# Kernel tuning notes

Measured on AMD Instinct MI355X. Metric: run time of the kernel, lower is better.

## Reference

```python
import jax, jax.numpy as jnp
import numpy as np

N, G, NG, E, P, D, H, L, MPD = 2048, 16, 128, 32768, 131072, 128, 4, 2, 5
EDI, EDH, IN_D, OUT_D, FFN = 16, 64, 64, 64, 512


def setup_inputs() -> dict:
    key = jax.random.key(0)
    ks = iter(jax.random.split(key, 64))
    nk = lambda: next(ks)
    # edges: endpoints within the same graph block
    ge = jnp.arange(E) // (E // G)
    edge_index = jnp.stack([
        ge * NG + jax.random.randint(nk(), (E,), 0, NG),
        ge * NG + jax.random.randint(nk(), (E,), 0, NG)]).astype(jnp.int32)
    # unique (src,dst) pairs per graph (flattened edge_paths dict)
    PG = P // G
    perm = jax.vmap(lambda k: jax.random.permutation(k, NG * NG)[:PG])(
        jax.random.split(nk(), G))  # [G,PG]
    off = (jnp.arange(G) * NG)[:, None]
    path_src = (off + perm // NG).reshape(-1).astype(jnp.int32)
    path_dst = (off + perm % NG).reshape(-1).astype(jnp.int32)
    gp = jnp.arange(P) // PG
    path_edges = (gp[:, None] * (E // G)
                  + jax.random.randint(nk(), (P, MPD), 0, E // G)).astype(jnp.int32)
    path_lens = jax.random.randint(nk(), (P,), 1, MPD + 1).astype(jnp.int32)
    ptr = (jnp.arange(G + 1) * NG).astype(jnp.int32)
    r = lambda shape, s=1.0: jax.random.normal(nk(), shape, jnp.float32) * s
    return dict(
        x=r((N, IN_D)), edge_attr=r((E, EDI)),
        edge_index=edge_index, path_src=path_src, path_dst=path_dst,
        path_edges=path_edges, path_lens=path_lens, ptr=ptr,
        W_in=r((IN_D, D), 0.1), b_in=jnp.zeros((D,)),
        W_ein=r((EDI, EDH), 0.1), b_ein=jnp.zeros((EDH,)),
        z_in=r((64, D), 0.02), z_out=r((64, D), 0.02),
        b_spatial=r((MPD,)),
        ln1_g=jnp.ones((L, D)), ln1_b=jnp.zeros((L, D)),
        Wq=r((L, H, D, D), 0.05), bq=jnp.zeros((L, H, D)),
        Wk=r((L, H, D, D), 0.05), bk=jnp.zeros((L, H, D)),
        Wv=r((L, H, D, D), 0.05), bv=jnp.zeros((L, H, D)),
        edge_vec=r((L, H, MPD, EDH), 0.1),
        Wo=r((L, H * D, D), 0.05), bo=jnp.zeros((L, D)),
        ln2_g=jnp.ones((L, D)), ln2_b=jnp.zeros((L, D)),
        W_f1=r((L, D, FFN), 0.05), b_f1=jnp.zeros((L, FFN)),
        W_f2=r((L, FFN, D), 0.05), b_f2=jnp.zeros((L, D)),
        W_out=r((D, OUT_D), 0.05), b_out=jnp.zeros((OUT_D,)),
    )


def _ln(x, g, b, eps=1e-5):
    m = jnp.mean(x, -1, keepdims=True)
    v = jnp.mean((x - m) ** 2, -1, keepdims=True)
    return (x - m) / jnp.sqrt(v + eps) * g + b


def _graphormer(x, edge_attr, W_in, b_in, W_ein, b_ein, z_in, z_out, b_spatial,
                ln1_g, ln1_b, Wq, bq, Wk, bk, Wv, bv, edge_vec, Wo, bo,
                ln2_g, ln2_b, W_f1, b_f1, W_f2, b_f2, W_out, b_out,
                edge_index, path_src, path_dst, path_edges, path_lens, ptr):
    n = x.shape[0]
    x = x @ W_in + b_in                      # node input projection
    ea = edge_attr @ W_ein + b_ein           # edge input projection
    # centrality encoding (degrees clipped to max-1)
    in_deg = jnp.minimum(jnp.zeros((n,), jnp.int32).at[edge_index[1]].add(1), z_in.shape[0] - 1)
    out_deg = jnp.minimum(jnp.zeros((n,), jnp.int32).at[edge_index[0]].add(1), z_out.shape[0] - 1)
    x = x + z_in[in_deg] + z_out[out_deg]
    # spatial encoding matrix b[src,dst] = b_spatial[min(len, MPD)-1]
    mpd = b_spatial.shape[0]
    bmat = jnp.zeros((n, n), x.dtype).at[path_src, path_dst].set(
        b_spatial[jnp.minimum(path_lens, mpd) - 1])
    # block-diagonal batch masks from ptr
    gids = jnp.searchsorted(ptr, jnp.arange(n), side='right') - 1
    block = gids[:, None] == gids[None, :]
    mask_neg = jnp.where(block, 1.0, -1e6).astype(x.dtype)
    mask_zero = block.astype(x.dtype)
    pe = ea[path_edges]                      # [P,MPD,EDH] gathered path edge feats
    pos_mask = (jnp.arange(mpd)[None, :] < path_lens[:, None]).astype(x.dtype)
    lens_f = path_lens.astype(x.dtype)
    nl, d = Wq.shape[0], x.shape[1]
    scale = jnp.sqrt(jnp.asarray(d, x.dtype))
    for l in range(nl):
        xn = _ln(x, ln1_g[l], ln1_b[l])
        q = jnp.einsum('nd,hde->hne', xn, Wq[l]) + bq[l][:, None, :]
        k = jnp.einsum('nd,hde->hne', xn, Wk[l]) + bk[l][:, None, :]
        v = jnp.einsum('nd,hde->hne', xn, Wv[l]) + bv[l][:, None, :]
        # per-head edge encoding: mean over path of <edge_vec[i], edge_attr[path[i]]>
        dots = jnp.einsum('hme,pme->hpm', edge_vec[l], pe)   # [H,P,MPD]
        vals = jnp.nan_to_num((dots * pos_mask).sum(-1) / lens_f)  # [H,P]
        c = jnp.zeros((vals.shape[0], n, n), x.dtype).at[:, path_src, path_dst].set(vals)
        a = jnp.einsum('hne,hme->hnm', q, k) / scale
        a = a * mask_zero                     # compute_a only fills diagonal blocks
        a = (a + bmat[None] + c) * mask_neg[None]
        sm = jax.nn.softmax(a, axis=-1) * mask_zero[None]
        o = jnp.einsum('hnm,hme->hne', sm, v)  # [H,N,D]
        o = jnp.transpose(o, (1, 0, 2)).reshape(n, -1) @ Wo[l] + bo[l]
        x = o + x
        x2 = _ln(x, ln2_g[l], ln2_b[l])
        x = (jax.nn.gelu(x2 @ W_f1[l] + b_f1[l], approximate=False) @ W_f2[l] + b_f2[l]) + x
    return x @ W_out + b_out


def reference(x, edge_attr, edge_index, path_src, path_dst, path_edges, path_lens, ptr,
              W_in, b_in, W_ein, b_ein, z_in, z_out, b_spatial,
              ln1_g, ln1_b, Wq, bq, Wk, bk, Wv, bv, edge_vec, Wo, bo,
              ln2_g, ln2_b, W_f1, b_f1, W_f2, b_f2, W_out, b_out):
    return _graphormer(x, edge_attr, W_in, b_in, W_ein, b_ein, z_in, z_out, b_spatial,
                       ln1_g, ln1_b, Wq, bq, Wk, bk, Wv, bv, edge_vec, Wo, bo,
                       ln2_g, ln2_b, W_f1, b_f1, W_f2, b_f2, W_out, b_out,
                       edge_index, path_src, path_dst, path_edges, path_lens, ptr)
```

## Files before the change

### kernel.cpp

```cpp
#include <hip/hip_runtime.h>
#include <math.h>

static constexpr int N_ = 2048, NG_ = 128, E_ = 32768, P_ = 131072,
  D_ = 128, H_ = 4, L_ = 2, MPD_ = 5, EDI_ = 16, EDH_ = 64,
  IND_ = 64, OUTD_ = 64, FFN_ = 512;

__global__ void k_deg(const int* __restrict__ ei, int* __restrict__ din, int* __restrict__ dou) {
  int e = blockIdx.x * blockDim.x + threadIdx.x;
  if (e < E_) {
    atomicAdd(&dou[ei[e]], 1);
    atomicAdd(&din[ei[E_ + e]], 1);
  }
}

__global__ void k_nodeproj(const float* __restrict__ x_in, const float* __restrict__ W,
                           const float* __restrict__ b, const float* __restrict__ z_in,
                           const float* __restrict__ z_out, const int* __restrict__ din,
                           const int* __restrict__ dou, float* __restrict__ x) {
  int n = blockIdx.x;
  int d = threadIdx.x;
  __shared__ float xs[IND_];
  if (d < IND_) xs[d] = x_in[n * IND_ + d];
  __syncthreads();
  float acc = b[d];
  for (int i = 0; i < IND_; ++i) acc += xs[i] * W[i * D_ + d];
  int di = min(din[n], 63), dz = min(dou[n], 63);
  acc += z_in[di * D_ + d] + z_out[dz * D_ + d];
  x[n * D_ + d] = acc;
}

__global__ void k_eproj(const float* __restrict__ ein, const float* __restrict__ W,
                        const float* __restrict__ b, float* __restrict__ ea) {
  int idx = blockIdx.x * blockDim.x + threadIdx.x;
  int e = idx >> 6, c = idx & 63;
  const float* row = ein + e * EDI_;
  float acc = b[c];
  for (int i = 0; i < EDI_; ++i) acc += row[i] * W[i * EDH_ + c];
  ea[idx] = acc;
}

static constexpr int ED_PAD = EDH_ + 4;
__global__ __launch_bounds__(256)
void k_edot2(const float* __restrict__ evec, const float* __restrict__ ea,
             float* __restrict__ edot) {
  __shared__ float eas[64][ED_PAD];
  __shared__ float evs[40][ED_PAD];
  int t = threadIdx.x;
  int e0 = blockIdx.x * 64;
  for (int i = t; i < 64 * (EDH_ / 4); i += 256) {
    int r = i >> 4, c = (i & 15) << 2;
    float4 v = *(const float4*)(ea + (size_t)(e0 + r) * EDH_ + c);
    *(float4*)&eas[r][c] = v;
  }
  for (int i = t; i < 40 * (EDH_ / 4); i += 256) {
    int r = i >> 4, c = (i & 15) << 2;
    float4 v = *(const float4*)(evec + (size_t)r * EDH_ + c);
    *(float4*)&evs[r][c] = v;
  }
  __syncthreads();
  int le = t & 63;
  int s0 = t >> 6;
  float acc[10];
  for (int ss = 0; ss < 10; ++ss) acc[ss] = 0.f;
  for (int i = 0; i < EDH_; i += 4) {
    float4 a = *(const float4*)&eas[le][i];
    for (int ss = 0; ss < 10; ++ss) {
      float4 b = *(const float4*)&evs[s0 + ss * 4][i];
      acc[ss] += a.x * b.x + a.y * b.y + a.z * b.z + a.w * b.w;
    }
  }
  for (int ss = 0; ss < 10; ++ss)
    edot[(size_t)(s0 + ss * 4) * E_ + e0 + le] = acc[ss];
}

__global__ void k_scatter(const int* __restrict__ psrc, const int* __restrict__ pdst,
                          const int* __restrict__ pedg, const int* __restrict__ plen,
                          const float* __restrict__ bsp, const float* __restrict__ edot_l,
                          float* __restrict__ bias) {
  int idx = blockIdx.x * blockDim.x + threadIdx.x;
  if (idx >= P_ * H_) return;
  int p = idx >> 2, h = idx & 3;
  int len = plen[p];
  int src = psrc[p];
  int dst = pdst[p] & (NG_ - 1);
  float acc = 0.f;
  for (int m = 0; m < MPD_; ++m)
    if (m < len) acc += edot_l[(h * MPD_ + m) * E_ + pedg[p * MPD_ + m]];
  float val = acc / (float)len + bsp[len - 1];
  bias[(h * N_ + src) * NG_ + dst] = val;
}

__global__ void k_ln(const float* __restrict__ x, const float* __restrict__ g,
                     const float* __restrict__ b, float* __restrict__ out) {
  int n = blockIdx.x;
  int d = threadIdx.x;
  float v = x[n * D_ + d];
  __shared__ float red[D_];
  red[d] = v; __syncthreads();
  for (int s = 64; s > 0; s >>= 1) { if (d < s) red[d] += red[d + s]; __syncthreads(); }
  float mean = red[0] * (1.0f / D_);
  __syncthreads();
  float c = v - mean;
  red[d] = c * c; __syncthreads();
  for (int s = 64; s > 0; s >>= 1) { if (d < s) red[d] += red[d + s]; __syncthreads(); }
  float var = red[0] * (1.0f / D_);
  out[n * D_ + d] = c * rsqrtf(var + 1e-5f) * g[d] + b[d];
}

static constexpr int QKV_ROWS = 8;
__global__ void k_qkv(const float* __restrict__ xn,
                      const float* __restrict__ Wq, const float* __restrict__ bq,
                      const float* __restrict__ Wk, const float* __restrict__ bk,
                      const float* __restrict__ Wv, const float* __restrict__ bv,
                      float* __restrict__ q, float* __restrict__ k, float* __restrict__ v) {
  int rb = blockIdx.x;
  int mh = blockIdx.y;
  int mat = mh >> 2, h = mh & 3;
  int e = threadIdx.x;
  const float* W  = (mat == 0 ? Wq : mat == 1 ? Wk : Wv) + h * D_ * D_;
  const float* bb = (mat == 0 ? bq : mat == 1 ? bk : bv) + h * D_;
  float* out      = (mat == 0 ? q  : mat == 1 ? k  : v)  + h * N_ * D_;
  __shared__ float xs[QKV_ROWS][D_];
  int n0 = rb * QKV_ROWS;
  for (int r = 0; r < QKV_ROWS; ++r) xs[r][e] = xn[(n0 + r) * D_ + e];
  __syncthreads();
  float acc[QKV_ROWS];
  float bvv = bb[e];
  for (int r = 0; r < QKV_ROWS; ++r) acc[r] = bvv;
  for (int d0 = 0; d0 < D_; d0 += 4) {
    float w0 = W[(d0 + 0) * D_ + e];
    float w1 = W[(d0 + 1) * D_ + e];
    float w2 = W[(d0 + 2) * D_ + e];
    float w3 = W[(d0 + 3) * D_ + e];
    for (int r = 0; r < QKV_ROWS; ++r) {
      float4 xv = *(const float4*)&xs[r][d0];
      acc[r] += xv.x * w0 + xv.y * w1 + xv.z * w2 + xv.w * w3;
    }
  }
  for (int r = 0; r < QKV_ROWS; ++r) out[(n0 + r) * D_ + e] = acc[r];
}

__global__ __launch_bounds__(256, 2)
void k_attn2(const float* __restrict__ q, const float* __restrict__ k,
             const float* __restrict__ v, const float* __restrict__ bias,
             float* __restrict__ o) {
  int bx = blockIdx.x;
  int h  = bx >> 8;
  int n0 = (bx & 255) * 8;
  int g0 = n0 & ~(NG_ - 1);
  int t  = threadIdx.x;
  int j    = t & 127;
  int half = t >> 7;
  int r0   = half * 4;

  __shared__ float Ks[NG_][D_ + 1];
  __shared__ float Qs[8][D_];
  __shared__ float Ps[8][NG_];
  __shared__ float rinv[8];

  const float* kbase = k + (size_t)(h * N_ + g0) * D_;
  for (int i = t; i < NG_ * D_ / 4; i += 256) {
    int r = i >> 5, c = (i & 31) << 2;
    float4 kv = *(const float4*)(kbase + r * D_ + c);
    Ks[r][c] = kv.x; Ks[r][c + 1] = kv.y; Ks[r][c + 2] = kv.z; Ks[r][c + 3] = kv.w;
  }
  const float* qbase = q + (size_t)(h * N_ + n0) * D_;
  for (int i = t; i < 8 * D_; i += 256) Qs[i >> 7][i & 127] = qbase[i];
  __syncthreads();

  const float* bb = bias + (size_t)(h * N_ + n0) * NG_;
  float s0 = 0.f, s1 = 0.f, s2 = 0.f, s3 = 0.f;
  for (int d0 = 0; d0 < D_; ++d0) {
    float kk = Ks[j][d0];
    s0 += Qs[r0 + 0][d0] * kk;
    s1 += Qs[r0 + 1][d0] * kk;
    s2 += Qs[r0 + 2][d0] * kk;
    s3 += Qs[r0 + 3][d0] * kk;
  }
  const float sc = 0.088388347648318447f;
  Ps[r0 + 0][j] = s0 * sc + bb[(r0 + 0) * NG_ + j];
  Ps[r0 + 1][j] = s1 * sc + bb[(r0 + 1) * NG_ + j];
  Ps[r0 + 2][j] = s2 * sc + bb[(r0 + 2) * NG_ + j];
  Ps[r0 + 3][j] = s3 * sc + bb[(r0 + 3) * NG_ + j];
  __syncthreads();

  int rr = t >> 5, c0 = t & 31;
  float a0 = Ps[rr][c0], a1 = Ps[rr][c0 + 32], a2 = Ps[rr][c0 + 64], a3 = Ps[rr][c0 + 96];
  float lm = fmaxf(fmaxf(a0, a1), fmaxf(a2, a3));
  for (int off = 16; off > 0; off >>= 1) lm = fmaxf(lm, __shfl_xor(lm, off, 32));
  float m = fmaxf(lm, 0.0f);
  float e0 = expf(a0 - m), e1 = expf(a1 - m), e2 = expf(a2 - m), e3 = expf(a3 - m);
  Ps[rr][c0] = e0; Ps[rr][c0 + 32] = e1; Ps[rr][c0 + 64] = e2; Ps[rr][c0 + 96] = e3;
  float ls = e0 + e1 + e2 + e3;
  for (int off = 16; off > 0; off >>= 1) ls += __shfl_xor(ls, off, 32);
  if (c0 == 0) rinv[rr] = 1.0f / (ls + (float)(N_ - NG_) * expf(-m));
  __syncthreads();

  const float* vbase = v + (size_t)(h * N_ + g0) * D_;
  float o0 = 0.f, o1 = 0.f, o2 = 0.f, o3 = 0.f;
  for (int jj = 0; jj < NG_; ++jj) {
    float vv = vbase[jj * D_ + j];
    float p0 = Ps[r0 + 0][jj], p1 = Ps[r0 + 1][jj], p2 = Ps[r0 + 2][jj], p3 = Ps[r0 + 3][jj];
    o0 += p0 * vv; o1 += p1 * vv; o2 += p2 * vv; o3 += p3 * vv;
  }
  float* ob = o + (size_t)(h * N_ + n0) * D_;
  ob[(r0 + 0) * D_ + j] = o0 * rinv[r0 + 0];
  ob[(r0 + 1) * D_ + j] = o1 * rinv[r0 + 1];
  ob[(r0 + 2) * D_ + j] = o2 * rinv[r0 + 2];
  ob[(r0 + 3) * D_ + j] = o3 * rinv[r0 + 3];
}

static constexpr int OP_ROWS = 8;
__global__ __launch_bounds__(128)
void k_oproj(const float* __restrict__ o, const float* __restrict__ Wo,
             const float* __restrict__ bo, float* __restrict__ x) {
  int n0 = blockIdx.x * OP_ROWS;
  int h  = blockIdx.y;
  int d = threadIdx.x;
  __shared__ float os[OP_ROWS][D_];
  for (int r = 0; r < OP_ROWS; ++r)
    os[r][d] = o[(size_t)(h * N_ + n0 + r) * D_ + d];
  __syncthreads();
  float acc[OP_ROWS];
  float bb = (h == 0) ? bo[d] : 0.0f;
  for (int r = 0; r < OP_ROWS; ++r) acc[r] = bb;
  const float* W = Wo + (size_t)h * D_ * D_;
  for (int k0 = 0; k0 < D_; k0 += 4) {
    float w0 = W[(k0 + 0) * D_ + d];
    float w1 = W[(k0 + 1) * D_ + d];
    float w2 = W[(k0 + 2) * D_ + d];
    float w3 = W[(k0 + 3) * D_ + d];
    for (int r = 0; r < OP_ROWS; ++r) {
      float4 ov = *(const float4*)&os[r][k0];
      acc[r] += ov.x * w0 + ov.y * w1 + ov.z * w2 + ov.w * w3;
    }
  }
  for (int r = 0; r < OP_ROWS; ++r)
    atomicAdd(&x[(size_t)(n0 + r) * D_ + d], acc[r]);
}

static constexpr int F1_ROWS = 8;
__global__ void k_ffn1(const float* __restrict__ x2, const float* __restrict__ W1,
                       const float* __restrict__ b1, float* __restrict__ h1) {
  int n0 = blockIdx.x * F1_ROWS;
  int f = blockIdx.y * 256 + threadIdx.x;
  __shared__ float xs[F1_ROWS][D_];
  for (int i = threadIdx.x; i < F1_ROWS * D_; i += 256)
    xs[i / D_][i % D_] = x2[(n0 + i / D_) * D_ + (i % D_)];
  __syncthreads();
  float acc[F1_ROWS];
  float bb = b1[f];
  for (int r = 0; r < F1_ROWS; ++r) acc[r] = bb;
  for (int d0 = 0; d0 < D_; d0 += 4) {
    float w0 = W1[(d0 + 0) * FFN_ + f];
    float w1 = W1[(d0 + 1) * FFN_ + f];
    float w2 = W1[(d0 + 2) * FFN_ + f];
    float w3 = W1[(d0 + 3) * FFN_ + f];
    for (int r = 0; r < F1_ROWS; ++r) {
      float4 xv = *(const float4*)&xs[r][d0];
      acc[r] += xv.x * w0 + xv.y * w1 + xv.z * w2 + xv.w * w3;
    }
  }
  for (int r = 0; r < F1_ROWS; ++r) {
    float u = acc[r];
    h1[(size_t)(n0 + r) * FFN_ + f] = 0.5f * u * (1.0f + erff(u * 0.70710678118654752440f));
  }
}

__global__ __launch_bounds__(128)
void k_ffn2(const float* __restrict__ h1, const float* __restrict__ W2,
            const float* __restrict__ b2, float* __restrict__ x) {
  int n0 = blockIdx.x * OP_ROWS;
  int c  = blockIdx.y;
  int d = threadIdx.x;
  int kb = c * 128;
  __shared__ float hs[OP_ROWS][128];
  for (int r = 0; r < OP_ROWS; ++r)
    hs[r][d] = h1[(size_t)(n0 + r) * FFN_ + kb + d];
  __syncthreads();
  float acc[OP_ROWS];
  float bb = (c == 0) ? b2[d] : 0.0f;
  for (int r = 0; r < OP_ROWS; ++r) acc[r] = bb;
  const float* W = W2 + (size_t)kb * D_;
  for (int k0 = 0; k0 < 128; k0 += 4) {
    float w0 = W[(k0 + 0) * D_ + d];
    float w1 = W[(k0 + 1) * D_ + d];
    float w2 = W[(k0 + 2) * D_ + d];
    float w3 = W[(k0 + 3) * D_ + d];
    for (int r = 0; r < OP_ROWS; ++r) {
      float4 hv = *(const float4*)&hs[r][k0];
      acc[r] += hv.x * w0 + hv.y * w1 + hv.z * w2 + hv.w * w3;
    }
  }
  for (int r = 0; r < OP_ROWS; ++r)
    atomicAdd(&x[(size_t)(n0 + r) * D_ + d], acc[r]);
}

__global__ void k_out(const float* __restrict__ x, const float* __restrict__ W,
                      const float* __restrict__ b, float* __restrict__ out) {
  int n = blockIdx.x;
  int c = threadIdx.x;
  __shared__ float xs[D_];
  xs[c] = x[n * D_ + c];
  xs[c + 64] = x[n * D_ + c + 64];
  __syncthreads();
  float acc = b[c];
  for (int d0 = 0; d0 < D_; ++d0) acc += xs[d0] * W[d0 * OUTD_ + c];
  out[n * OUTD_ + c] = acc;
}

extern "C" void kernel_launch(void* const* d_in, const int* in_sizes, int n_in,
                              void* d_out, int out_size, void* d_ws, size_t ws_size,
                              hipStream_t stream) {
  const float* x_in      = (const float*)d_in[0];
  const float* edge_attr = (const float*)d_in[1];
  const int*   edge_index= (const int*)  d_in[2];
  const int*   path_src  = (const int*)  d_in[3];
  const int*   path_dst  = (const int*)  d_in[4];
  const int*   path_edges= (const int*)  d_in[5];
  const int*   path_lens = (const int*)  d_in[6];
  const float* W_in  = (const float*)d_in[8];
  const float* b_in  = (const float*)d_in[9];
  const float* W_ein = (const float*)d_in[10];
  const float* b_ein = (const float*)d_in[11];
  const float* z_in  = (const float*)d_in[12];
  const float* z_out = (const float*)d_in[13];
  const float* b_sp  = (const float*)d_in[14];
  const float* ln1_g = (const float*)d_in[15];
  const float* ln1_b = (const float*)d_in[16];
  const float* Wq    = (const float*)d_in[17];
  const float* bq    = (const float*)d_in[18];
  const float* Wk    = (const float*)d_in[19];
  const float* bk    = (const float*)d_in[20];
  const float* Wv    = (const float*)d_in[21];
  const float* bv    = (const float*)d_in[22];
  const float* evec  = (const float*)d_in[23];
  const float* Wo    = (const float*)d_in[24];
  const float* bo    = (const float*)d_in[25];
  const float* ln2_g = (const float*)d_in[26];
  const float* ln2_b = (const float*)d_in[27];
  const float* W_f1  = (const float*)d_in[28];
  const float* b_f1  = (const float*)d_in[29];
  const float* W_f2  = (const float*)d_in[30];
  const float* b_f2  = (const float*)d_in[31];
  const float* W_out = (const float*)d_in[32];
  const float* b_out = (const float*)d_in[33];
  float* out = (float*)d_out;

  char* wp = (char*)d_ws;
  auto alloc = [&](size_t bytes) { void* p = wp; wp += (bytes + 255) & ~(size_t)255; return p; };
  int*   deg_in  = (int*)  alloc(N_ * 4);
  int*   deg_out = (int*)  alloc(N_ * 4);
  float* x    = (float*)alloc((size_t)N_ * D_ * 4);
  float* ea   = (float*)alloc((size_t)E_ * EDH_ * 4);
  float* edot = (float*)alloc((size_t)L_ * H_ * MPD_ * E_ * 4);
  float* bias = (float*)alloc((size_t)H_ * N_ * NG_ * 4);
  float* xn   = (float*)alloc((size_t)N_ * D_ * 4);
  float* q    = (float*)alloc((size_t)H_ * N_ * D_ * 4);
  float* k    = (float*)alloc((size_t)H_ * N_ * D_ * 4);
  float* v    = (float*)alloc((size_t)H_ * N_ * D_ * 4);
  float* o    = (float*)alloc((size_t)H_ * N_ * D_ * 4);
  float* x2   = (float*)alloc((size_t)N_ * D_ * 4);
  float* h1   = (float*)alloc((size_t)N_ * FFN_ * 4);

  hipMemsetAsync(deg_in, 0, 2 * N_ * 4, stream);
  k_deg<<<E_ / 256, 256, 0, stream>>>(edge_index, deg_in, deg_out);
  k_nodeproj<<<N_, D_, 0, stream>>>(x_in, W_in, b_in, z_in, z_out, deg_in, deg_out, x);
  k_eproj<<<(E_ * EDH_) / 256, 256, 0, stream>>>(edge_attr, W_ein, b_ein, ea);
  k_edot2<<<E_ / 64, 256, 0, stream>>>(evec, ea, edot);

  for (int l = 0; l < L_; ++l) {
    k_ln<<<N_, D_, 0, stream>>>(x, ln1_g + l * D_, ln1_b + l * D_, xn);
    {
      dim3 g(N_ / QKV_ROWS, 3 * H_);
      k_qkv<<<g, D_, 0, stream>>>(xn,
          Wq + (size_t)l * H_ * D_ * D_, bq + (size_t)l * H_ * D_,
          Wk + (size_t)l * H_ * D_ * D_, bk + (size_t)l * H_ * D_,
          Wv + (size_t)l * H_ * D_ * D_, bv + (size_t)l * H_ * D_,
          q, k, v);
    }
    hipMemsetAsync(bias, 0, (size_t)H_ * N_ * NG_ * 4, stream);
    k_scatter<<<(P_ * H_) / 256, 256, 0, stream>>>(path_src, path_dst, path_edges, path_lens,
        b_sp, edot + (size_t)l * H_ * MPD_ * E_, bias);
    k_attn2<<<H_ * (N_ / 8), 256, 0, stream>>>(q, k, v, bias, o);
    {
      dim3 g(N_ / OP_ROWS, H_);
      k_oproj<<<g, D_, 0, stream>>>(o, Wo + (size_t)l * H_ * D_ * D_, bo + l * D_, x);
    }
    k_ln<<<N_, D_, 0, stream>>>(x, ln2_g + l * D_, ln2_b + l * D_, x2);
    {
      dim3 g(N_ / F1_ROWS, FFN_ / 256);
      k_ffn1<<<g, 256, 0, stream>>>(x2, W_f1 + (size_t)l * D_ * FFN_, b_f1 + l * FFN_, h1);
    }
    {
      dim3 g(N_ / OP_ROWS, FFN_ / 128);
      k_ffn2<<<g, D_, 0, stream>>>(h1, W_f2 + (size_t)l * FFN_ * D_, b_f2 + l * D_, x);
    }
  }
  k_out<<<N_, OUTD_, 0, stream>>>(x, W_out, b_out, out);
}
```

Before: 395.8 us.

## Fuse layernorms into QKV and FFN1 kernels; loop heads in path scatter

Removes the standalone layernorm kernels by computing row mean/variance with shuffle reductions inside the QKV and FFN1 kernels and normalizing in shared memory. This drops four launches and the xn/x2 round trips through global memory. In exchange, layernorm work is recomputed redundantly across the 12 QKV blocks and 2 FFN1 blocks that share a row group. The path scatter kernel now uses one thread per path looping over heads, so path edge indices are loaded once per path instead of once per head.

```diff
diff --git a/kernel.cpp b/kernel.cpp
--- a/kernel.cpp
+++ b/kernel.cpp
@@ -77,38 +77,25 @@
                           const int* __restrict__ pedg, const int* __restrict__ plen,
                           const float* __restrict__ bsp, const float* __restrict__ edot_l,
                           float* __restrict__ bias) {
-  int idx = blockIdx.x * blockDim.x + threadIdx.x;
-  if (idx >= P_ * H_) return;
-  int p = idx >> 2, h = idx & 3;
+  int p = blockIdx.x * blockDim.x + threadIdx.x;
+  if (p >= P_) return;
   int len = plen[p];
   int src = psrc[p];
   int dst = pdst[p] & (NG_ - 1);
-  float acc = 0.f;
-  for (int m = 0; m < MPD_; ++m)
-    if (m < len) acc += edot_l[(h * MPD_ + m) * E_ + pedg[p * MPD_ + m]];
-  float val = acc / (float)len + bsp[len - 1];
-  bias[(h * N_ + src) * NG_ + dst] = val;
-}
-
-__global__ void k_ln(const float* __restrict__ x, const float* __restrict__ g,
-                     const float* __restrict__ b, float* __restrict__ out) {
-  int n = blockIdx.x;
-  int d = threadIdx.x;
-  float v = x[n * D_ + d];
-  __shared__ float red[D_];
-  red[d] = v; __syncthreads();
-  for (int s = 64; s > 0; s >>= 1) { if (d < s) red[d] += red[d + s]; __syncthreads(); }
-  float mean = red[0] * (1.0f / D_);
-  __syncthreads();
-  float c = v - mean;
-  red[d] = c * c; __syncthreads();
-  for (int s = 64; s > 0; s >>= 1) { if (d < s) red[d] += red[d + s]; __syncthreads(); }
-  float var = red[0] * (1.0f / D_);
-  out[n * D_ + d] = c * rsqrtf(var + 1e-5f) * g[d] + b[d];
+  int ei[MPD_];
+  for (int m = 0; m < MPD_; ++m) ei[m] = pedg[p * MPD_ + m];
+  float bs = bsp[len - 1];
+  for (int h = 0; h < H_; ++h) {
+    float acc = 0.f;
+    for (int m = 0; m < MPD_; ++m)
+      if (m < len) acc += edot_l[(size_t)(h * MPD_ + m) * E_ + ei[m]];
+    bias[(size_t)(h * N_ + src) * NG_ + dst] = acc / (float)len + bs;
+  }
 }
 
 static constexpr int QKV_ROWS = 8;
-__global__ void k_qkv(const float* __restrict__ xn,
+__global__ void k_qkv(const float* __restrict__ x,
+                      const float* __restrict__ lg, const float* __restrict__ lb,
                       const float* __restrict__ Wq, const float* __restrict__ bq,
                       const float* __restrict__ Wk, const float* __restrict__ bk,
                       const float* __restrict__ Wv, const float* __restrict__ bv,
@@ -121,8 +108,24 @@
   const float* bb = (mat == 0 ? bq : mat == 1 ? bk : bv) + h * D_;
   float* out      = (mat == 0 ? q  : mat == 1 ? k  : v)  + h * N_ * D_;
   __shared__ float xs[QKV_ROWS][D_];
+  __shared__ float mu[QKV_ROWS], rstd[QKV_ROWS];
   int n0 = rb * QKV_ROWS;
-  for (int r = 0; r < QKV_ROWS; ++r) xs[r][e] = xn[(n0 + r) * D_ + e];
+  for (int r = 0; r < QKV_ROWS; ++r) xs[r][e] = x[(n0 + r) * D_ + e];
+  __syncthreads();
+  {
+    int rr = e >> 4, l16 = e & 15;
+    float s = 0.f;
+    for (int i = 0; i < 8; ++i) s += xs[rr][l16 + 16 * i];
+    for (int m = 1; m < 16; m <<= 1) s += __shfl_xor(s, m, 16);
+    float mean = s * (1.0f / D_);
+    float vv = 0.f;
+    for (int i = 0; i < 8; ++i) { float c = xs[rr][l16 + 16 * i] - mean; vv += c * c; }
+    for (int m = 1; m < 16; m <<= 1) vv += __shfl_xor(vv, m, 16);
+    if (l16 == 0) { mu[rr] = mean; rstd[rr] = rsqrtf(vv * (1.0f / D_) + 1e-5f); }
+  }
+  __syncthreads();
+  float gg = lg[e], gb = lb[e];
+  for (int r = 0; r < QKV_ROWS; ++r) xs[r][e] = (xs[r][e] - mu[r]) * rstd[r] * gg + gb;
   __syncthreads();
   float acc[QKV_ROWS];
   float bvv = bb[e];
@@ -240,16 +243,37 @@
 }
 
 static constexpr int F1_ROWS = 8;
-__global__ void k_ffn1(const float* __restrict__ x2, const float* __restrict__ W1,
-                       const float* __restrict__ b1, float* __restrict__ h1) {
+__global__ void k_ffn1(const float* __restrict__ x,
+                       const float* __restrict__ lg, const float* __restrict__ lb,
+                       const float* __restrict__ W1, const float* __restrict__ bf1,
+                       float* __restrict__ h1) {
   int n0 = blockIdx.x * F1_ROWS;
   int f = blockIdx.y * 256 + threadIdx.x;
+  int t = threadIdx.x;
   __shared__ float xs[F1_ROWS][D_];
-  for (int i = threadIdx.x; i < F1_ROWS * D_; i += 256)
-    xs[i / D_][i % D_] = x2[(n0 + i / D_) * D_ + (i % D_)];
+  __shared__ float mu[F1_ROWS], rstd[F1_ROWS];
+  for (int i = t; i < F1_ROWS * D_; i += 256)
+    xs[i >> 7][i & 127] = x[(size_t)(n0 + (i >> 7)) * D_ + (i & 127)];
+  __syncthreads();
+  {
+    int rr = t >> 5, l32 = t & 31;
+    float s = 0.f;
+    for (int i = 0; i < 4; ++i) s += xs[rr][l32 + 32 * i];
+    for (int m = 1; m < 32; m <<= 1) s += __shfl_xor(s, m, 32);
+    float mean = s * (1.0f / D_);
+    float vv = 0.f;
+    for (int i = 0; i < 4; ++i) { float c = xs[rr][l32 + 32 * i] - mean; vv += c * c; }
+    for (int m = 1; m < 32; m <<= 1) vv += __shfl_xor(vv, m, 32);
+    if (l32 == 0) { mu[rr] = mean; rstd[rr] = rsqrtf(vv * (1.0f / D_) + 1e-5f); }
+  }
+  __syncthreads();
+  for (int i = t; i < F1_ROWS * D_; i += 256) {
+    int r = i >> 7, d = i & 127;
+    xs[r][d] = (xs[r][d] - mu[r]) * rstd[r] * lg[d] + lb[d];
+  }
   __syncthreads();
   float acc[F1_ROWS];
-  float bb = b1[f];
+  float bb = bf1[f];
   for (int r = 0; r < F1_ROWS; ++r) acc[r] = bb;
   for (int d0 = 0; d0 < D_; d0 += 4) {
     float w0 = W1[(d0 + 0) * FFN_ + f];
@@ -355,12 +379,10 @@
   float* ea   = (float*)alloc((size_t)E_ * EDH_ * 4);
   float* edot = (float*)alloc((size_t)L_ * H_ * MPD_ * E_ * 4);
   float* bias = (float*)alloc((size_t)H_ * N_ * NG_ * 4);
-  float* xn   = (float*)alloc((size_t)N_ * D_ * 4);
   float* q    = (float*)alloc((size_t)H_ * N_ * D_ * 4);
   float* k    = (float*)alloc((size_t)H_ * N_ * D_ * 4);
   float* v    = (float*)alloc((size_t)H_ * N_ * D_ * 4);
   float* o    = (float*)alloc((size_t)H_ * N_ * D_ * 4);
-  float* x2   = (float*)alloc((size_t)N_ * D_ * 4);
   float* h1   = (float*)alloc((size_t)N_ * FFN_ * 4);
 
   hipMemsetAsync(deg_in, 0, 2 * N_ * 4, stream);
@@ -370,27 +392,26 @@
   k_edot2<<<E_ / 64, 256, 0, stream>>>(evec, ea, edot);
 
   for (int l = 0; l < L_; ++l) {
-    k_ln<<<N_, D_, 0, stream>>>(x, ln1_g + l * D_, ln1_b + l * D_, xn);
     {
       dim3 g(N_ / QKV_ROWS, 3 * H_);
-      k_qkv<<<g, D_, 0, stream>>>(xn,
+      k_qkv<<<g, D_, 0, stream>>>(x, ln1_g + l * D_, ln1_b + l * D_,
           Wq + (size_t)l * H_ * D_ * D_, bq + (size_t)l * H_ * D_,
           Wk + (size_t)l * H_ * D_ * D_, bk + (size_t)l * H_ * D_,
           Wv + (size_t)l * H_ * D_ * D_, bv + (size_t)l * H_ * D_,
           q, k, v);
     }
     hipMemsetAsync(bias, 0, (size_t)H_ * N_ * NG_ * 4, stream);
-    k_scatter<<<(P_ * H_) / 256, 256, 0, stream>>>(path_src, path_dst, path_edges, path_lens,
+    k_scatter<<<P_ / 256, 256, 0, stream>>>(path_src, path_dst, path_edges, path_lens,
         b_sp, edot + (size_t)l * H_ * MPD_ * E_, bias);
     k_attn2<<<H_ * (N_ / 8), 256, 0, stream>>>(q, k, v, bias, o);
     {
       dim3 g(N_ / OP_ROWS, H_);
       k_oproj<<<g, D_, 0, stream>>>(o, Wo + (size_t)l * H_ * D_ * D_, bo + l * D_, x);
     }
-    k_ln<<<N_, D_, 0, stream>>>(x, ln2_g + l * D_, ln2_b + l * D_, x2);
     {
       dim3 g(N_ / F1_ROWS, FFN_ / 256);
-      k_ffn1<<<g, 256, 0, stream>>>(x2, W_f1 + (size_t)l * D_ * FFN_, b_f1 + l * FFN_, h1);
+      k_ffn1<<<g, 256, 0, stream>>>(x, ln2_g + l * D_, ln2_b + l * D_,
+          W_f1 + (size_t)l * D_ * FFN_, b_f1 + l * FFN_, h1);
     }
     {
       dim3 g(N_ / OP_ROWS, FFN_ / 128);
```

Measured after the change: 389.2 us. Within noise of the previous version (-1.7%).
